# Kernel optimization log

Measured on AMD Instinct MI355X. Metric: run time of the kernel, lower is better.

The kernel has to match this reference:

```python
import jax, jax.numpy as jnp
import numpy as np

KERNEL_SIZE = 4


def setup_inputs() -> dict:
    key = jax.random.key(0)
    k1, k2 = jax.random.split(key)
    B, L, D, K = 4, 4096, 2048, KERNEL_SIZE
    inputs = jax.random.normal(k1, (B, L, D), dtype=jnp.float32)
    # torch init: zeros with last tap = 1 (identity). Use random weights for a
    # non-trivial correctness baseline; same shape (D, 1, K) as the nn.Parameter.
    weight = jax.random.normal(k2, (D, 1, K), dtype=jnp.float32) * 0.1
    return {"inputs": inputs, "weight": weight}


def _causal_dw_conv(inputs, weight):
    # inputs: (B, L, D); weight: (D, 1, K)
    K = weight.shape[-1]
    D = weight.shape[0]
    # Stay in NLC layout (avoids the torch transpose/pad/transpose passes).
    # lax depthwise conv: kernel layout WIO with feature_group_count=D -> (K, 1, D)
    kern = jnp.transpose(weight, (2, 1, 0))  # (K, 1, D)
    out = jax.lax.conv_general_dilated(
        inputs, kern,
        window_strides=(1,),
        padding=((K - 1, 0),),  # causal: left-pad K-1 zeros
        dimension_numbers=("NWC", "WIO", "NWC"),
        feature_group_count=D,
    )
    return out  # (B, L, D)


def reference(inputs, weight):
    mixed = _causal_dw_conv(inputs, weight)
    return jax.nn.silu(mixed)
```

## Files before the change

kernel.cpp:

```cpp
#include <hip/hip_runtime.h>
#include <math.h>


#define LT 16
#define TPB 256

__device__ __forceinline__ float silu(float v) {
    return v / (1.0f + __expf(-v));
}

__global__ __launch_bounds__(TPB) void CausalDepthwiseConv1d_9543417332015_kernel(
    const float* __restrict__ x,
    const float* __restrict__ w,
    float* __restrict__ out,
    int L, int D4) {
    const int d4 = blockIdx.x * TPB + threadIdx.x;
    const int l0 = blockIdx.y * LT;
    const int b  = blockIdx.z;

    const float4* __restrict__ x4 =
        reinterpret_cast<const float4*>(x) + (size_t)b * L * D4;
    float4* __restrict__ o4 =
        reinterpret_cast<float4*>(out) + (size_t)b * L * D4;
    const float4* __restrict__ w4 = reinterpret_cast<const float4*>(w);

    const float4 wa = w4[d4 * 4 + 0];
    const float4 wb = w4[d4 * 4 + 1];
    const float4 wc = w4[d4 * 4 + 2];
    const float4 wd = w4[d4 * 4 + 3];
    const float4 w0 = make_float4(wa.x, wb.x, wc.x, wd.x);
    const float4 w1 = make_float4(wa.y, wb.y, wc.y, wd.y);
    const float4 w2 = make_float4(wa.z, wb.z, wc.z, wd.z);
    const float4 w3 = make_float4(wa.w, wb.w, wc.w, wd.w);

    const float4 zero = make_float4(0.f, 0.f, 0.f, 0.f);
    float4 xm3 = (l0 >= 3) ? x4[(size_t)(l0 - 3) * D4 + d4] : zero;
    float4 xm2 = (l0 >= 2) ? x4[(size_t)(l0 - 2) * D4 + d4] : zero;
    float4 xm1 = (l0 >= 1) ? x4[(size_t)(l0 - 1) * D4 + d4] : zero;

#pragma unroll
    for (int i = 0; i < LT; ++i) {
        const size_t row = (size_t)(l0 + i) * D4 + d4;
        const float4 xc = x4[row];
        float4 a;
        a.x = w0.x * xm3.x + w1.x * xm2.x + w2.x * xm1.x + w3.x * xc.x;
        a.y = w0.y * xm3.y + w1.y * xm2.y + w2.y * xm1.y + w3.y * xc.y;
        a.z = w0.z * xm3.z + w1.z * xm2.z + w2.z * xm1.z + w3.z * xc.z;
        a.w = w0.w * xm3.w + w1.w * xm2.w + w2.w * xm1.w + w3.w * xc.w;
        a.x = silu(a.x);
        a.y = silu(a.y);
        a.z = silu(a.z);
        a.w = silu(a.w);
        o4[row] = a;
        xm3 = xm2;
        xm2 = xm1;
        xm1 = xc;
    }
}

extern "C" void kernel_launch(void* const* d_in, const int* in_sizes, int n_in,
                              void* d_out, int out_size, void* d_ws, size_t ws_size,
                              hipStream_t stream) {
    const float* x = (const float*)d_in[0];
    const float* w = (const float*)d_in[1];
    float* out = (float*)d_out;

    const int K = 4;
    const int D = in_sizes[1] / K;
    const int L = 4096;
    const int B = in_sizes[0] / (L * D);
    const int D4 = D / 4;

    dim3 grid(D4 / TPB, L / LT, B);
    dim3 block(TPB);
    CausalDepthwiseConv1d_9543417332015_kernel<<<grid, block, 0, stream>>>(
        x, w, out, L, D4);
}
```

Baseline: 240.5 us.

## Switch to float2 per thread with batched row loads and shorter L tiles

```diff
diff --git a/kernel.cpp b/kernel.cpp
--- a/kernel.cpp
+++ b/kernel.cpp
@@ -2,59 +2,51 @@
 #include <math.h>
 
 
-#define LT 16
+#define LT 8
 #define TPB 256
 
 __device__ __forceinline__ float silu(float v) {
     return v / (1.0f + __expf(-v));
 }
 
-__global__ __launch_bounds__(TPB) void CausalDepthwiseConv1d_9543417332015_kernel(
+__global__ __launch_bounds__(TPB, 8) void CausalDepthwiseConv1d_9543417332015_kernel(
     const float* __restrict__ x,
     const float* __restrict__ w,
     float* __restrict__ out,
-    int L, int D4) {
-    const int d4 = blockIdx.x * TPB + threadIdx.x;
+    int L, int D2) {
+    const int d2 = blockIdx.x * TPB + threadIdx.x;
     const int l0 = blockIdx.y * LT;
     const int b  = blockIdx.z;
 
-    const float4* __restrict__ x4 =
-        reinterpret_cast<const float4*>(x) + (size_t)b * L * D4;
-    float4* __restrict__ o4 =
-        reinterpret_cast<float4*>(out) + (size_t)b * L * D4;
+    const float2* __restrict__ x2 =
+        reinterpret_cast<const float2*>(x) + (size_t)b * L * D2;
+    float2* __restrict__ o2 =
+        reinterpret_cast<float2*>(out) + (size_t)b * L * D2;
     const float4* __restrict__ w4 = reinterpret_cast<const float4*>(w);
 
-    const float4 wa = w4[d4 * 4 + 0];
-    const float4 wb = w4[d4 * 4 + 1];
-    const float4 wc = w4[d4 * 4 + 2];
-    const float4 wd = w4[d4 * 4 + 3];
-    const float4 w0 = make_float4(wa.x, wb.x, wc.x, wd.x);
-    const float4 w1 = make_float4(wa.y, wb.y, wc.y, wd.y);
-    const float4 w2 = make_float4(wa.z, wb.z, wc.z, wd.z);
-    const float4 w3 = make_float4(wa.w, wb.w, wc.w, wd.w);
+    const float4 wa = w4[2 * d2 + 0];
+    const float4 wb = w4[2 * d2 + 1];
 
-    const float4 zero = make_float4(0.f, 0.f, 0.f, 0.f);
-    float4 xm3 = (l0 >= 3) ? x4[(size_t)(l0 - 3) * D4 + d4] : zero;
-    float4 xm2 = (l0 >= 2) ? x4[(size_t)(l0 - 2) * D4 + d4] : zero;
-    float4 xm1 = (l0 >= 1) ? x4[(size_t)(l0 - 1) * D4 + d4] : zero;
+    float2 r[LT + 3];
+    const float2 zero = make_float2(0.f, 0.f);
+    if (l0 >= 3) {
+#pragma unroll
+        for (int i = 0; i < LT + 3; ++i)
+            r[i] = x2[(size_t)(l0 - 3 + i) * D2 + d2];
+    } else {
+#pragma unroll
+        for (int i = 0; i < LT + 3; ++i)
+            r[i] = (l0 - 3 + i >= 0) ? x2[(size_t)(l0 - 3 + i) * D2 + d2] : zero;
+    }
 
 #pragma unroll
     for (int i = 0; i < LT; ++i) {
-        const size_t row = (size_t)(l0 + i) * D4 + d4;
-        const float4 xc = x4[row];
-        float4 a;
-        a.x = w0.x * xm3.x + w1.x * xm2.x + w2.x * xm1.x + w3.x * xc.x;
-        a.y = w0.y * xm3.y + w1.y * xm2.y + w2.y * xm1.y + w3.y * xc.y;
-        a.z = w0.z * xm3.z + w1.z * xm2.z + w2.z * xm1.z + w3.z * xc.z;
-        a.w = w0.w * xm3.w + w1.w * xm2.w + w2.w * xm1.w + w3.w * xc.w;
+        float2 a;
+        a.x = wa.x * r[i].x + wa.y * r[i + 1].x + wa.z * r[i + 2].x + wa.w * r[i + 3].x;
+        a.y = wb.x * r[i].y + wb.y * r[i + 1].y + wb.z * r[i + 2].y + wb.w * r[i + 3].y;
         a.x = silu(a.x);
         a.y = silu(a.y);
-        a.z = silu(a.z);
-        a.w = silu(a.w);
-        o4[row] = a;
-        xm3 = xm2;
-        xm2 = xm1;
-        xm1 = xc;
+        o2[(size_t)(l0 + i) * D2 + d2] = a;
     }
 }
 
@@ -69,10 +61,10 @@
     const int D = in_sizes[1] / K;
     const int L = 4096;
     const int B = in_sizes[0] / (L * D);
-    const int D4 = D / 4;
+    const int D2 = D / 2;
 
-    dim3 grid(D4 / TPB, L / LT, B);
+    dim3 grid(D2 / TPB, L / LT, B);
     dim3 block(TPB);
     CausalDepthwiseConv1d_9543417332015_kernel<<<grid, block, 0, stream>>>(
-        x, w, out, L, D4);
+        x, w, out, L, D2);
 }
```

Measured after the change: 229.6 us. 1.05x faster.
